# Optimization experiments

Measured on AMD Instinct MI355X. Metric: run time of the kernel, lower is better.

The kernel has to match this reference:

```python
import jax, jax.numpy as jnp
import numpy as np

N_NODES = 50000
N_EDGES = 1600000
IN_DIM = 128
HID = 128
SHARED = 64
N_GRAPHS = 2048


def setup_inputs() -> dict:
    key = jax.random.key(0)
    ks = jax.random.split(key, 16)
    x = jax.random.normal(ks[0], (N_NODES, IN_DIM), dtype=jnp.float32)
    edge_index = jax.random.randint(ks[1], (2, N_EDGES), 0, N_NODES, dtype=jnp.int64)
    batch = jnp.sort(jax.random.randint(ks[2], (N_NODES,), 0, N_GRAPHS, dtype=jnp.int64))

    def lin(k, fan_in, fan_out):
        bound = 1.0 / np.sqrt(fan_in)
        kw, kb = jax.random.split(k)
        W = jax.random.uniform(kw, (fan_in, fan_out), minval=-bound, maxval=bound, dtype=jnp.float32)
        b = jax.random.uniform(kb, (fan_out,), minval=-bound, maxval=bound, dtype=jnp.float32)
        return W, b

    W1a, b1a = lin(ks[3], IN_DIM, HID)
    W1b, b1b = lin(ks[4], HID, HID)
    W2a, b2a = lin(ks[5], HID, HID)
    W2b, b2b = lin(ks[6], HID, HID)
    Ws, bs = lin(ks[7], HID, SHARED)
    WlS, blS = lin(ks[8], SHARED, 1)
    WlP, blP = lin(ks[9], SHARED, 1)
    WnR, bnR = lin(ks[10], SHARED, 1)
    return dict(x=x, edge_index=edge_index, batch=batch,
                W1a=W1a, b1a=b1a, W1b=W1b, b1b=b1b,
                W2a=W2a, b2a=b2a, W2b=W2b, b2b=b2b,
                Ws=Ws, bs=bs, WlS=WlS, blS=blS, WlP=WlP, blP=blP, WnR=WnR, bnR=bnR)


def gin_conv(x, src, dst, Wa, ba, Wb, bb):
    # GINConv (eps=0): h_i = MLP(x_i + sum_{j->i} x_j)
    agg = jax.ops.segment_sum(x[src], dst, num_segments=N_NODES)
    h = x + agg
    h = jax.nn.relu(h @ Wa + ba)
    return h @ Wb + bb


def reference(x, edge_index, batch, W1a, b1a, W1b, b1b, W2a, b2a, W2b, b2b,
              Ws, bs, WlS, blS, WlP, blP, WnR, bnR):
    src, dst = edge_index[0], edge_index[1]
    h = jax.nn.relu(gin_conv(x, src, dst, W1a, b1a, W1b, b1b))
    h = jax.nn.relu(gin_conv(h, src, dst, W2a, b2a, W2b, b2b))
    # global mean pool over graph ids
    sums = jax.ops.segment_sum(h, batch, num_segments=N_GRAPHS)
    counts = jax.ops.segment_sum(jnp.ones((h.shape[0],), h.dtype), batch, num_segments=N_GRAPHS)
    pooled = sums / jnp.maximum(counts, 1.0)[:, None]
    g = jax.nn.relu(pooled @ Ws + bs)
    out_logS = (g @ WlS + blS)[:, 0]
    out_logP = (g @ WlP + blP)[:, 0]
    out_NR = (g @ WnR + bnR)[:, 0]
    return (out_logS, out_logP, out_NR)
```

## Files before the change

kernel.cpp:

```cpp
#include <hip/hip_runtime.h>
#include <hip/hip_bf16.h>


#define IN_DIM 128
#define NFINE 128
#define BIN_EPB 4096
#define SRCCH 16
#define NSLOT 6400
#define SPT 13

typedef float  f32x4  __attribute__((ext_vector_type(4)));
typedef short  bf16x4 __attribute__((ext_vector_type(4)));
typedef short  bf16x8 __attribute__((ext_vector_type(8)));

__device__ __forceinline__ unsigned short bf16_rne(float v) {
    unsigned u = __float_as_uint(v);
    unsigned t = u + 0x7fffu + ((u >> 16) & 1u);
    return (unsigned short)(t >> 16);
}


__global__ __launch_bounds__(256) void f32_to_bf16_kernel(
    const float4* __restrict__ in, uint4* __restrict__ out, int n8)
{
    int i = blockIdx.x * 256 + threadIdx.x;
    if (i >= n8) return;
    float4 a = in[i * 2];
    float4 b = in[i * 2 + 1];
    float v[8] = {a.x, a.y, a.z, a.w, b.x, b.y, b.z, b.w};
    unsigned r[4];
#pragma unroll
    for (int j = 0; j < 4; ++j)
        r[j] = (unsigned)bf16_rne(v[j * 2]) | ((unsigned)bf16_rne(v[j * 2 + 1]) << 16);
    out[i] = make_uint4(r[0], r[1], r[2], r[3]);
}


__global__ __launch_bounds__(256) void conv_weights_kernel(
    const float* __restrict__ W0, const float* __restrict__ W1,
    const float* __restrict__ W2, const float* __restrict__ W3,
    unsigned short* __restrict__ Wh, unsigned short* __restrict__ Wl)
{
    int m   = blockIdx.x >> 6;
    int idx = (blockIdx.x & 63) * 256 + threadIdx.x;
    const float* W = (m == 0) ? W0 : (m == 1) ? W1 : (m == 2) ? W2 : W3;
    int k = idx >> 7, n = idx & 127;
    float v = W[idx];
    unsigned short hh = bf16_rne(v);
    float hf = __uint_as_float(((unsigned)hh) << 16);
    unsigned short ll = bf16_rne(v - hf);
    Wh[m * 16384 + n * 128 + k] = hh;
    Wl[m * 16384 + n * 128 + k] = ll;
}


__global__ __launch_bounds__(256) void bin_kernel(
    const int* __restrict__ src, const int* __restrict__ dst,
    int2* __restrict__ buckets, int* __restrict__ bcur,
    int n_edges, int n_nodes, int cap)
{
    __shared__ int cnt[NFINE];
    __shared__ int base[NFINE];
    for (int i = threadIdx.x; i < NFINE; i += 256) cnt[i] = 0;
    __syncthreads();

    const int e0 = blockIdx.x * BIN_EPB + threadIdx.x * 16;
    int ne = n_edges - e0;
    if (ne < 0) ne = 0;
    if (ne > 16) ne = 16;

    int d[16], s[16], off[16];
    if (ne == 16) {
#pragma unroll
        for (int q = 0; q < 4; ++q) {
            int4 dv = *(const int4*)(dst + e0 + q * 4);
            int4 sv = *(const int4*)(src + e0 + q * 4);
            d[q * 4 + 0] = dv.x; d[q * 4 + 1] = dv.y;
            d[q * 4 + 2] = dv.z; d[q * 4 + 3] = dv.w;
            s[q * 4 + 0] = sv.x; s[q * 4 + 1] = sv.y;
            s[q * 4 + 2] = sv.z; s[q * 4 + 3] = sv.w;
        }
    } else {
#pragma unroll
        for (int j = 0; j < 16; ++j) {
            d[j] = (j < ne) ? dst[e0 + j] : 0;
            s[j] = (j < ne) ? src[e0 + j] : 0;
        }
    }
#pragma unroll
    for (int j = 0; j < 16; ++j)
        if (j < ne) {
            int b = (int)(((long long)d[j] * NFINE) / n_nodes);
            off[j] = atomicAdd(&cnt[b], 1);
        }
    __syncthreads();
    for (int i = threadIdx.x; i < NFINE; i += 256)
        base[i] = atomicAdd(&bcur[i], cnt[i]);
    __syncthreads();
#pragma unroll
    for (int j = 0; j < 16; ++j)
        if (j < ne) {
            int b = (int)(((long long)d[j] * NFINE) / n_nodes);
            buckets[(size_t)b * cap + base[b] + off[j]] = make_int2(d[j], s[j]);
        }
}

__global__ __launch_bounds__(512) void csr_fused_kernel(
    const int2* __restrict__ buckets, const int* __restrict__ bcnt,
    int* __restrict__ row_start, int* __restrict__ csr_src,
    int cap, int n_nodes, int n_edges)
{
    __shared__ int bc[NFINE];
    __shared__ int h[NSLOT];
    __shared__ int tsum[512];
    __shared__ int bbase_s;

    const int b = blockIdx.x;
    const int t = threadIdx.x;
    const int lo_n = (int)(((long long)b * n_nodes + NFINE - 1) / NFINE);
    const int hi_n = (int)(((long long)(b + 1) * n_nodes + NFINE - 1) / NFINE);
    const int sl = hi_n - lo_n;

    if (t < NFINE) bc[t] = bcnt[t];
    for (int i = t; i < NSLOT; i += 512) h[i] = 0;
    __syncthreads();
    if (t == 0) {
        int s = 0;
        for (int i = 0; i < b; ++i) s += bc[i];
        bbase_s = s;
    }
    const int nb = bc[b];
    const int2* bp = buckets + (size_t)b * cap;
    __syncthreads();

    for (int i = t; i < nb; i += 512) {
        int2 e = bp[i];
        int key = (e.x - lo_n) * SRCCH + (int)(((long long)e.y * SRCCH) / n_nodes);
        atomicAdd(&h[key], 1);
    }
    __syncthreads();

    int base = 0;
#pragma unroll
    for (int j = 0; j < SPT; ++j) {
        int slot = t * SPT + j;
        if (slot < NSLOT) {
            int v = h[slot];
            h[slot] = base;
            base += v;
        }
    }
    tsum[t] = base;
    __syncthreads();
    for (int off = 1; off < 512; off <<= 1) {
        int tmp = (t >= off) ? tsum[t - off] : 0;
        __syncthreads();
        tsum[t] += tmp;
        __syncthreads();
    }
    int texcl = tsum[t] - base + bbase_s;
#pragma unroll
    for (int j = 0; j < SPT; ++j) {
        int slot = t * SPT + j;
        if (slot < NSLOT) h[slot] += texcl;
    }
    __syncthreads();
    for (int i = t; i < sl; i += 512) row_start[lo_n + i] = h[i * SRCCH];
    if (b == NFINE - 1 && t == 0) row_start[n_nodes] = n_edges;
    __syncthreads();

    for (int i = t; i < nb; i += 512) {
        int2 e = bp[i];
        int key = (e.x - lo_n) * SRCCH + (int)(((long long)e.y * SRCCH) / n_nodes);
        csr_src[atomicAdd(&h[key], 1)] = e.y;
    }
}

#define HSTRIDE 132

__device__ __forceinline__ void add_row8(float acc[8], uint4 r) {
    union { unsigned u; float f; } c;
    c.u = r.x << 16;         acc[0] += c.f;
    c.u = r.x & 0xffff0000u; acc[1] += c.f;
    c.u = r.y << 16;         acc[2] += c.f;
    c.u = r.y & 0xffff0000u; acc[3] += c.f;
    c.u = r.z << 16;         acc[4] += c.f;
    c.u = r.z & 0xffff0000u; acc[5] += c.f;
    c.u = r.w << 16;         acc[6] += c.f;
    c.u = r.w & 0xffff0000u; acc[7] += c.f;
}

template <int LAYER>
__global__ __launch_bounds__(512) void fused_gin_layer_kernel(
    const float* __restrict__ xf,
    const uint4* __restrict__ selfh,
    const uint4* __restrict__ selfl,
    const uint4* __restrict__ nbr,
    const int* __restrict__ row_start, const int* __restrict__ csr_src,
    const unsigned short* __restrict__ Wa_h, const unsigned short* __restrict__ Wa_l,
    const float* __restrict__ ba,
    const unsigned short* __restrict__ Wb_h, const unsigned short* __restrict__ Wb_l,
    const float* __restrict__ bb,
    float* __restrict__ C, unsigned short* __restrict__ Ch,
    unsigned short* __restrict__ Cl, int M)
{
    __shared__ __align__(16) unsigned short Hh[64][HSTRIDE];
    __shared__ __align__(16) unsigned short Hl[64][HSTRIDE];

    const int t    = threadIdx.x;
    const int brow = blockIdx.x * 64;

    {
        const int lane = t & 15;
        const int gr   = t >> 4;
#pragma unroll
        for (int it = 0; it < 2; ++it) {
            const int rl   = it * 32 + gr;
            const int node = brow + rl;
            float acc[8] = {0.f, 0.f, 0.f, 0.f, 0.f, 0.f, 0.f, 0.f};
            if (node < M) {
                if constexpr (LAYER == 1) {
                    const f32x4* xfr = (const f32x4*)(xf + (size_t)node * IN_DIM + lane * 8);
                    f32x4 a0 = xfr[0];
                    f32x4 a1 = xfr[1];
                    acc[0] = a0.x; acc[1] = a0.y; acc[2] = a0.z; acc[3] = a0.w;
                    acc[4] = a1.x; acc[5] = a1.y; acc[6] = a1.z; acc[7] = a1.w;
                } else {
                    add_row8(acc, selfh[(size_t)node * 16 + lane]);
                    add_row8(acc, selfl[(size_t)node * 16 + lane]);
                }
                const int lo = row_start[node];
                const int hi = row_start[node + 1];
                int e = lo;
                for (; e + 3 < hi; e += 4) {
                    int s0 = csr_src[e];
                    int s1 = csr_src[e + 1];
                    int s2 = csr_src[e + 2];
                    int s3 = csr_src[e + 3];
                    uint4 r0 = nbr[(size_t)s0 * 16 + lane];
                    uint4 r1 = nbr[(size_t)s1 * 16 + lane];
                    uint4 r2 = nbr[(size_t)s2 * 16 + lane];
                    uint4 r3 = nbr[(size_t)s3 * 16 + lane];
                    add_row8(acc, r0);
                    add_row8(acc, r1);
                    add_row8(acc, r2);
                    add_row8(acc, r3);
                }
                for (; e < hi; ++e)
                    add_row8(acc, nbr[(size_t)csr_src[e] * 16 + lane]);
            }
            unsigned short hh[8], ll[8];
#pragma unroll
            for (int j = 0; j < 8; ++j) {
                unsigned short h = bf16_rne(acc[j]);
                hh[j] = h;
                ll[j] = bf16_rne(acc[j] - __uint_as_float(((unsigned)h) << 16));
            }
            *(bf16x4*)&Hh[rl][lane * 8]     = *(const bf16x4*)&hh[0];
            *(bf16x4*)&Hh[rl][lane * 8 + 4] = *(const bf16x4*)&hh[4];
            *(bf16x4*)&Hl[rl][lane * 8]     = *(const bf16x4*)&ll[0];
            *(bf16x4*)&Hl[rl][lane * 8 + 4] = *(const bf16x4*)&ll[4];
        }
    }
    __syncthreads();

    const int wave = t >> 6;
    const int lane = t & 63;
    const int l15  = lane & 15;
    const int quad = lane >> 4;
    const int rh   = (wave & 1) * 32;
    const int cq   = (wave >> 1) * 32;

    f32x4 acc[2][2];
#pragma unroll
    for (int ti = 0; ti < 2; ++ti)
#pragma unroll
        for (int ct = 0; ct < 2; ++ct) acc[ti][ct] = {0.f, 0.f, 0.f, 0.f};

#pragma unroll
    for (int k0 = 0; k0 < IN_DIM; k0 += 32) {
        const int hk = k0 + quad * 8;
        bf16x8 ah[2], al[2];
#pragma unroll
        for (int ti = 0; ti < 2; ++ti) {
            const int hr = rh + ti * 16 + l15;
            bf16x4 h0 = *(const bf16x4*)&Hh[hr][hk];
            bf16x4 h1 = *(const bf16x4*)&Hh[hr][hk + 4];
            bf16x4 l0 = *(const bf16x4*)&Hl[hr][hk];
            bf16x4 l1 = *(const bf16x4*)&Hl[hr][hk + 4];
            ah[ti] = __builtin_shufflevector(h0, h1, 0, 1, 2, 3, 4, 5, 6, 7);
            al[ti] = __builtin_shufflevector(l0, l1, 0, 1, 2, 3, 4, 5, 6, 7);
        }
#pragma unroll
        for (int ct = 0; ct < 2; ++ct) {
            const size_t woff = (size_t)(cq + ct * 16 + l15) * IN_DIM + k0 + quad * 8;
            bf16x8 wh = *(const bf16x8*)(Wa_h + woff);
            bf16x8 wl = *(const bf16x8*)(Wa_l + woff);
            acc[0][ct] = __builtin_amdgcn_mfma_f32_16x16x32_bf16(ah[0], wh, acc[0][ct], 0, 0, 0);
            acc[1][ct] = __builtin_amdgcn_mfma_f32_16x16x32_bf16(ah[1], wh, acc[1][ct], 0, 0, 0);
            acc[0][ct] = __builtin_amdgcn_mfma_f32_16x16x32_bf16(al[0], wh, acc[0][ct], 0, 0, 0);
            acc[1][ct] = __builtin_amdgcn_mfma_f32_16x16x32_bf16(al[1], wh, acc[1][ct], 0, 0, 0);
            acc[0][ct] = __builtin_amdgcn_mfma_f32_16x16x32_bf16(ah[0], wl, acc[0][ct], 0, 0, 0);
            acc[1][ct] = __builtin_amdgcn_mfma_f32_16x16x32_bf16(ah[1], wl, acc[1][ct], 0, 0, 0);
        }
    }
    __syncthreads();

#pragma unroll
    for (int ti = 0; ti < 2; ++ti) {
#pragma unroll
        for (int ct = 0; ct < 2; ++ct) {
            int col = cq + ct * 16 + l15;
            float b = ba[col];
#pragma unroll
            for (int r = 0; r < 4; ++r) {
                int rl = rh + ti * 16 + quad * 4 + r;
                float v = fmaxf(acc[ti][ct][r] + b, 0.f);
                unsigned short hh = bf16_rne(v);
                Hh[rl][col] = hh;
                Hl[rl][col] = bf16_rne(v - __uint_as_float(((unsigned)hh) << 16));
            }
            acc[ti][ct] = {0.f, 0.f, 0.f, 0.f};
        }
    }
    __syncthreads();

#pragma unroll
    for (int k0 = 0; k0 < IN_DIM; k0 += 32) {
        const int hk = k0 + quad * 8;
        bf16x8 ah[2], al[2];
#pragma unroll
        for (int ti = 0; ti < 2; ++ti) {
            const int hr = rh + ti * 16 + l15;
            bf16x4 h0 = *(const bf16x4*)&Hh[hr][hk];
            bf16x4 h1 = *(const bf16x4*)&Hh[hr][hk + 4];
            bf16x4 l0 = *(const bf16x4*)&Hl[hr][hk];
            bf16x4 l1 = *(const bf16x4*)&Hl[hr][hk + 4];
            ah[ti] = __builtin_shufflevector(h0, h1, 0, 1, 2, 3, 4, 5, 6, 7);
            al[ti] = __builtin_shufflevector(l0, l1, 0, 1, 2, 3, 4, 5, 6, 7);
        }
#pragma unroll
        for (int ct = 0; ct < 2; ++ct) {
            const size_t woff = (size_t)(cq + ct * 16 + l15) * IN_DIM + k0 + quad * 8;
            bf16x8 wh = *(const bf16x8*)(Wb_h + woff);
            bf16x8 wl = *(const bf16x8*)(Wb_l + woff);
            acc[0][ct] = __builtin_amdgcn_mfma_f32_16x16x32_bf16(ah[0], wh, acc[0][ct], 0, 0, 0);
            acc[1][ct] = __builtin_amdgcn_mfma_f32_16x16x32_bf16(ah[1], wh, acc[1][ct], 0, 0, 0);
            acc[0][ct] = __builtin_amdgcn_mfma_f32_16x16x32_bf16(al[0], wh, acc[0][ct], 0, 0, 0);
            acc[1][ct] = __builtin_amdgcn_mfma_f32_16x16x32_bf16(al[1], wh, acc[1][ct], 0, 0, 0);
            acc[0][ct] = __builtin_amdgcn_mfma_f32_16x16x32_bf16(ah[0], wl, acc[0][ct], 0, 0, 0);
            acc[1][ct] = __builtin_amdgcn_mfma_f32_16x16x32_bf16(ah[1], wl, acc[1][ct], 0, 0, 0);
        }
    }

#pragma unroll
    for (int ti = 0; ti < 2; ++ti) {
        const int rbase = brow + rh + ti * 16 + quad * 4;
#pragma unroll
        for (int ct = 0; ct < 2; ++ct) {
            int col = cq + ct * 16 + l15;
            float b = bb[col];
#pragma unroll
            for (int r = 0; r < 4; ++r) {
                int row = rbase + r;
                if (row < M) {
                    float o = fmaxf(acc[ti][ct][r] + b, 0.f);
                    if constexpr (LAYER == 1) {
                        unsigned short hh = bf16_rne(o);
                        Ch[(size_t)row * IN_DIM + col] = hh;
                        Cl[(size_t)row * IN_DIM + col] =
                            bf16_rne(o - __uint_as_float(((unsigned)hh) << 16));
                    } else {
                        C[(size_t)row * IN_DIM + col] = o;
                    }
                }
            }
        }
    }
}


__device__ __forceinline__ int lower_bound_i(const int* __restrict__ a, int n, int v) {
    int lo = 0, hi = n;
    while (lo < hi) {
        int mid = (lo + hi) >> 1;
        if (a[mid] < v) lo = mid + 1; else hi = mid;
    }
    return lo;
}

__global__ __launch_bounds__(128) void pool_kernel(
    const float* __restrict__ h, const int* __restrict__ batch,
    float* __restrict__ pooled, int n_nodes, int n_graphs)
{
    int g = blockIdx.x;
    int lo = lower_bound_i(batch, n_nodes, g);
    int hi = lower_bound_i(batch, n_nodes, g + 1);
    int j = threadIdx.x;
    float acc = 0.f;
    for (int i = lo; i < hi; ++i)
        acc += h[(size_t)i * IN_DIM + j];
    float cnt = (float)(hi - lo);
    pooled[(size_t)g * IN_DIM + j] = acc / fmaxf(cnt, 1.0f);
}

__global__ __launch_bounds__(64) void head_kernel(
    const float* __restrict__ pooled,
    const float* __restrict__ Ws,  const float* __restrict__ bs,
    const float* __restrict__ WlS, const float* __restrict__ blS,
    const float* __restrict__ WlP, const float* __restrict__ blP,
    const float* __restrict__ WnR, const float* __restrict__ bnR,
    float* __restrict__ out, int n_graphs)
{
    int g = blockIdx.x;
    int j = threadIdx.x;
    const float* p = pooled + (size_t)g * IN_DIM;
    float acc = bs[j];
#pragma unroll 8
    for (int k = 0; k < IN_DIM; ++k)
        acc = fmaf(p[k], Ws[k * 64 + j], acc);
    float gj = fmaxf(acc, 0.f);
    float s1 = gj * WlS[j];
    float s2 = gj * WlP[j];
    float s3 = gj * WnR[j];
#pragma unroll
    for (int off = 32; off > 0; off >>= 1) {
        s1 += __shfl_down(s1, off);
        s2 += __shfl_down(s2, off);
        s3 += __shfl_down(s3, off);
    }
    if (j == 0) {
        out[g]                = s1 + blS[0];
        out[n_graphs + g]     = s2 + blP[0];
        out[2 * n_graphs + g] = s3 + bnR[0];
    }
}


extern "C" void kernel_launch(void* const* d_in, const int* in_sizes, int n_in,
                              void* d_out, int out_size, void* d_ws, size_t ws_size,
                              hipStream_t stream)
{
    const float* x   = (const float*)d_in[0];
    const int*   ei  = (const int*)d_in[1];
    const int*   bat = (const int*)d_in[2];
    const float* W1a = (const float*)d_in[3];
    const float* b1a = (const float*)d_in[4];
    const float* W1b = (const float*)d_in[5];
    const float* b1b = (const float*)d_in[6];
    const float* W2a = (const float*)d_in[7];
    const float* b2a = (const float*)d_in[8];
    const float* W2b = (const float*)d_in[9];
    const float* b2b = (const float*)d_in[10];
    const float* Ws  = (const float*)d_in[11];
    const float* bs  = (const float*)d_in[12];
    const float* WlS = (const float*)d_in[13];
    const float* blS = (const float*)d_in[14];
    const float* WlP = (const float*)d_in[15];
    const float* blP = (const float*)d_in[16];
    const float* WnR = (const float*)d_in[17];
    const float* bnR = (const float*)d_in[18];

    const int n_nodes  = in_sizes[0] / IN_DIM;
    const int n_edges  = in_sizes[1] / 2;
    const int n_graphs = out_size / 3;
    const int* src = ei;
    const int* dst = ei + n_edges;

    const size_t node_elems   = (size_t)n_nodes * IN_DIM;
    const size_t pooled_elems = (size_t)n_graphs * IN_DIM;

    unsigned short* xb = (unsigned short*)d_ws;
    unsigned short* Ch = xb + node_elems;
    unsigned short* Cl = Ch + node_elems;
    float* P3     = (float*)(Cl + node_elems);
    float* pooled = P3 + node_elems;
    int* row_start = (int*)(pooled + pooled_elems);
    int* bcur      = row_start + (n_nodes + 1);
    int* csr_src   = bcur + NFINE;
    unsigned short* wt_h = (unsigned short*)(csr_src + n_edges);
    unsigned short* wt_l = wt_h + 4 * 16384;

    const int cap = n_edges / NFINE + 2048;
    int2* buckets = (int2*)P3;

    const int layerblocks = (n_nodes + 63) / 64;
    const int binblocks = (n_edges + BIN_EPB - 1) / BIN_EPB;
    const int n8 = (int)(node_elems / 8);
    const int cvtblocks = (n8 + 255) / 256;

    conv_weights_kernel<<<256, 256, 0, stream>>>(W1a, W1b, W2a, W2b, wt_h, wt_l);
    hipMemsetAsync(bcur, 0, NFINE * sizeof(int), stream);
    bin_kernel<<<binblocks, 256, 0, stream>>>(src, dst, buckets, bcur,
                                              n_edges, n_nodes, cap);
    csr_fused_kernel<<<NFINE, 512, 0, stream>>>(buckets, bcur, row_start,
                                                csr_src, cap, n_nodes, n_edges);
    f32_to_bf16_kernel<<<cvtblocks, 256, 0, stream>>>((const float4*)x, (uint4*)xb, n8);

    fused_gin_layer_kernel<1><<<layerblocks, 512, 0, stream>>>(
        x, nullptr, nullptr, (const uint4*)xb, row_start, csr_src,
        wt_h, wt_l, b1a, wt_h + 16384, wt_l + 16384, b1b,
        nullptr, Ch, Cl, n_nodes);

    fused_gin_layer_kernel<2><<<layerblocks, 512, 0, stream>>>(
        nullptr, (const uint4*)Ch, (const uint4*)Cl, (const uint4*)Ch,
        row_start, csr_src,
        wt_h + 2 * 16384, wt_l + 2 * 16384, b2a,
        wt_h + 3 * 16384, wt_l + 3 * 16384, b2b,
        P3, nullptr, nullptr, n_nodes);

    pool_kernel<<<n_graphs, 128, 0, stream>>>(P3, bat, pooled, n_nodes, n_graphs);
    head_kernel<<<n_graphs, 64, 0, stream>>>(pooled, Ws, bs, WlS, blS, WlP, blP,
                                             WnR, bnR, (float*)d_out, n_graphs);
}
```

Baseline: 344.0 us.

## Fuse mean-pool into layer-2 epilogue, merge setup kernels, double CSR bins

Layer 2 no longer writes a full fp32 node-feature array. Each block stages its output tile in LDS and does segmented column sums over the sorted batch ids, then atomically adds those sums into a zeroed pooled buffer. The count division moves into the head kernel, which finds graph boundaries by binary search. The weight conversion, x-to-bf16 conversion and memset are merged into one setup kernel, and the CSR binning changes from 128 to 256 fine buckets with smaller histograms. This removes one large write/read round trip and two launches, at the cost of float atomics that can make results nondeterministic.

```diff
diff --git a/kernel.cpp b/kernel.cpp
--- a/kernel.cpp
+++ b/kernel.cpp
@@ -3,11 +3,11 @@
 
 
 #define IN_DIM 128
-#define NFINE 128
+#define NFINE 256
 #define BIN_EPB 4096
 #define SRCCH 16
-#define NSLOT 6400
-#define SPT 13
+#define NSLOT 3200
+#define SPT 7
 
 typedef float  f32x4  __attribute__((ext_vector_type(4)));
 typedef short  bf16x4 __attribute__((ext_vector_type(4)));
@@ -20,37 +20,38 @@
 }
 
 
-__global__ __launch_bounds__(256) void f32_to_bf16_kernel(
-    const float4* __restrict__ in, uint4* __restrict__ out, int n8)
-{
-    int i = blockIdx.x * 256 + threadIdx.x;
-    if (i >= n8) return;
-    float4 a = in[i * 2];
-    float4 b = in[i * 2 + 1];
-    float v[8] = {a.x, a.y, a.z, a.w, b.x, b.y, b.z, b.w};
-    unsigned r[4];
-#pragma unroll
-    for (int j = 0; j < 4; ++j)
-        r[j] = (unsigned)bf16_rne(v[j * 2]) | ((unsigned)bf16_rne(v[j * 2 + 1]) << 16);
-    out[i] = make_uint4(r[0], r[1], r[2], r[3]);
-}
-
-
-__global__ __launch_bounds__(256) void conv_weights_kernel(
+__global__ __launch_bounds__(256) void setup_kernel(
+    const float4* __restrict__ xin, uint4* __restrict__ xb, int n8,
     const float* __restrict__ W0, const float* __restrict__ W1,
     const float* __restrict__ W2, const float* __restrict__ W3,
-    unsigned short* __restrict__ Wh, unsigned short* __restrict__ Wl)
+    unsigned short* __restrict__ Wh, unsigned short* __restrict__ Wl,
+    int* __restrict__ bcur, float* __restrict__ pooled, int npool)
 {
-    int m   = blockIdx.x >> 6;
-    int idx = (blockIdx.x & 63) * 256 + threadIdx.x;
-    const float* W = (m == 0) ? W0 : (m == 1) ? W1 : (m == 2) ? W2 : W3;
-    int k = idx >> 7, n = idx & 127;
-    float v = W[idx];
-    unsigned short hh = bf16_rne(v);
-    float hf = __uint_as_float(((unsigned)hh) << 16);
-    unsigned short ll = bf16_rne(v - hf);
-    Wh[m * 16384 + n * 128 + k] = hh;
-    Wl[m * 16384 + n * 128 + k] = ll;
+    int gid = blockIdx.x * 256 + threadIdx.x;
+    if (gid < n8) {
+        float4 a = xin[gid * 2];
+        float4 b = xin[gid * 2 + 1];
+        float v[8] = {a.x, a.y, a.z, a.w, b.x, b.y, b.z, b.w};
+        unsigned r[4];
+#pragma unroll
+        for (int j = 0; j < 4; ++j)
+            r[j] = (unsigned)bf16_rne(v[j * 2]) | ((unsigned)bf16_rne(v[j * 2 + 1]) << 16);
+        xb[gid] = make_uint4(r[0], r[1], r[2], r[3]);
+    }
+    if (gid < 4 * 16384) {
+        int m   = gid >> 14;
+        int idx = gid & 16383;
+        const float* W = (m == 0) ? W0 : (m == 1) ? W1 : (m == 2) ? W2 : W3;
+        int k = idx >> 7, n = idx & 127;
+        float v = W[idx];
+        unsigned short hh = bf16_rne(v);
+        float hf = __uint_as_float(((unsigned)hh) << 16);
+        unsigned short ll = bf16_rne(v - hf);
+        Wh[m * 16384 + n * 128 + k] = hh;
+        Wl[m * 16384 + n * 128 + k] = ll;
+    }
+    if (gid < NFINE) bcur[gid] = 0;
+    if (gid < npool) pooled[gid] = 0.f;
 }
 
 
@@ -121,7 +122,7 @@
     const int hi_n = (int)(((long long)(b + 1) * n_nodes + NFINE - 1) / NFINE);
     const int sl = hi_n - lo_n;
 
-    if (t < NFINE) bc[t] = bcnt[t];
+    for (int i = t; i < NFINE; i += 512) bc[i] = bcnt[i];
     for (int i = t; i < NSLOT; i += 512) h[i] = 0;
     __syncthreads();
     if (t == 0) {
@@ -201,11 +202,13 @@
     const float* __restrict__ ba,
     const unsigned short* __restrict__ Wb_h, const unsigned short* __restrict__ Wb_l,
     const float* __restrict__ bb,
-    float* __restrict__ C, unsigned short* __restrict__ Ch,
-    unsigned short* __restrict__ Cl, int M)
+    unsigned short* __restrict__ Ch, unsigned short* __restrict__ Cl,
+    float* __restrict__ pooled, const int* __restrict__ batch, int M)
 {
-    __shared__ __align__(16) unsigned short Hh[64][HSTRIDE];
-    __shared__ __align__(16) unsigned short Hl[64][HSTRIDE];
+    __shared__ __align__(16) unsigned short LDSBUF[2][64][HSTRIDE];
+    __shared__ int sbatch[64];
+    auto& Hh = LDSBUF[0];
+    auto& Hl = LDSBUF[1];
 
     const int t    = threadIdx.x;
     const int brow = blockIdx.x * 64;
@@ -353,28 +356,65 @@
         }
     }
 
-#pragma unroll
-    for (int ti = 0; ti < 2; ++ti) {
-        const int rbase = brow + rh + ti * 16 + quad * 4;
-#pragma unroll
-        for (int ct = 0; ct < 2; ++ct) {
-            int col = cq + ct * 16 + l15;
-            float b = bb[col];
-#pragma unroll
-            for (int r = 0; r < 4; ++r) {
-                int row = rbase + r;
-                if (row < M) {
-                    float o = fmaxf(acc[ti][ct][r] + b, 0.f);
-                    if constexpr (LAYER == 1) {
+    if constexpr (LAYER == 1) {
+#pragma unroll
+        for (int ti = 0; ti < 2; ++ti) {
+            const int rbase = brow + rh + ti * 16 + quad * 4;
+#pragma unroll
+            for (int ct = 0; ct < 2; ++ct) {
+                int col = cq + ct * 16 + l15;
+                float b = bb[col];
+#pragma unroll
+                for (int r = 0; r < 4; ++r) {
+                    int row = rbase + r;
+                    if (row < M) {
+                        float o = fmaxf(acc[ti][ct][r] + b, 0.f);
                         unsigned short hh = bf16_rne(o);
                         Ch[(size_t)row * IN_DIM + col] = hh;
                         Cl[(size_t)row * IN_DIM + col] =
                             bf16_rne(o - __uint_as_float(((unsigned)hh) << 16));
-                    } else {
-                        C[(size_t)row * IN_DIM + col] = o;
                     }
                 }
             }
+        }
+    } else {
+        __syncthreads();
+        float* ftile = (float*)&LDSBUF[0][0][0];
+#pragma unroll
+        for (int ti = 0; ti < 2; ++ti) {
+#pragma unroll
+            for (int ct = 0; ct < 2; ++ct) {
+                int col = cq + ct * 16 + l15;
+                float b = bb[col];
+#pragma unroll
+                for (int r = 0; r < 4; ++r) {
+                    int rl = rh + ti * 16 + quad * 4 + r;
+                    ftile[rl * 128 + col] = fmaxf(acc[ti][ct][r] + b, 0.f);
+                }
+            }
+        }
+        if (t < 64) {
+            int node = brow + t;
+            sbatch[t] = (node < M) ? batch[node] : -1;
+        }
+        __syncthreads();
+        if (t < 128) {
+            const int col = t;
+            float run = 0.f;
+            int curg = sbatch[0];
+#pragma unroll 1
+            for (int r = 0; r < 64; ++r) {
+                int g = sbatch[r];
+                if (g != curg) {
+                    if (curg >= 0)
+                        atomicAdd(&pooled[(size_t)curg * IN_DIM + col], run);
+                    curg = g;
+                    run = 0.f;
+                }
+                if (g >= 0) run += ftile[r * 128 + col];
+            }
+            if (curg >= 0)
+                atomicAdd(&pooled[(size_t)curg * IN_DIM + col], run);
         }
     }
 }
@@ -389,23 +429,8 @@
     return lo;
 }
 
-__global__ __launch_bounds__(128) void pool_kernel(
-    const float* __restrict__ h, const int* __restrict__ batch,
-    float* __restrict__ pooled, int n_nodes, int n_graphs)
-{
-    int g = blockIdx.x;
-    int lo = lower_bound_i(batch, n_nodes, g);
-    int hi = lower_bound_i(batch, n_nodes, g + 1);
-    int j = threadIdx.x;
-    float acc = 0.f;
-    for (int i = lo; i < hi; ++i)
-        acc += h[(size_t)i * IN_DIM + j];
-    float cnt = (float)(hi - lo);
-    pooled[(size_t)g * IN_DIM + j] = acc / fmaxf(cnt, 1.0f);
-}
-
 __global__ __launch_bounds__(64) void head_kernel(
-    const float* __restrict__ pooled,
+    const float* __restrict__ pooled, const int* __restrict__ batch, int n_nodes,
     const float* __restrict__ Ws,  const float* __restrict__ bs,
     const float* __restrict__ WlS, const float* __restrict__ blS,
     const float* __restrict__ WlP, const float* __restrict__ blP,
@@ -414,12 +439,15 @@
 {
     int g = blockIdx.x;
     int j = threadIdx.x;
+    int lo = lower_bound_i(batch, n_nodes, g);
+    int hi = lower_bound_i(batch, n_nodes, g + 1);
+    float inv = 1.f / fmaxf((float)(hi - lo), 1.0f);
     const float* p = pooled + (size_t)g * IN_DIM;
-    float acc = bs[j];
+    float acc = 0.f;
 #pragma unroll 8
     for (int k = 0; k < IN_DIM; ++k)
         acc = fmaf(p[k], Ws[k * 64 + j], acc);
-    float gj = fmaxf(acc, 0.f);
+    float gj = fmaxf(acc * inv + bs[j], 0.f);
     float s1 = gj * WlS[j];
     float s2 = gj * WlP[j];
     float s3 = gj * WnR[j];
@@ -473,8 +501,7 @@
     unsigned short* xb = (unsigned short*)d_ws;
     unsigned short* Ch = xb + node_elems;
     unsigned short* Cl = Ch + node_elems;
-    float* P3     = (float*)(Cl + node_elems);
-    float* pooled = P3 + node_elems;
+    float* pooled = (float*)(Cl + node_elems);
     int* row_start = (int*)(pooled + pooled_elems);
     int* bcur      = row_start + (n_nodes + 1);
     int* csr_src   = bcur + NFINE;
@@ -482,34 +509,34 @@
     unsigned short* wt_l = wt_h + 4 * 16384;
 
     const int cap = n_edges / NFINE + 2048;
-    int2* buckets = (int2*)P3;
+    int2* buckets = (int2*)Ch;
 
     const int layerblocks = (n_nodes + 63) / 64;
     const int binblocks = (n_edges + BIN_EPB - 1) / BIN_EPB;
     const int n8 = (int)(node_elems / 8);
     const int cvtblocks = (n8 + 255) / 256;
 
-    conv_weights_kernel<<<256, 256, 0, stream>>>(W1a, W1b, W2a, W2b, wt_h, wt_l);
-    hipMemsetAsync(bcur, 0, NFINE * sizeof(int), stream);
+    setup_kernel<<<cvtblocks, 256, 0, stream>>>(
+        (const float4*)x, (uint4*)xb, n8, W1a, W1b, W2a, W2b,
+        wt_h, wt_l, bcur, pooled, (int)pooled_elems);
     bin_kernel<<<binblocks, 256, 0, stream>>>(src, dst, buckets, bcur,
                                               n_edges, n_nodes, cap);
     csr_fused_kernel<<<NFINE, 512, 0, stream>>>(buckets, bcur, row_start,
                                                 csr_src, cap, n_nodes, n_edges);
-    f32_to_bf16_kernel<<<cvtblocks, 256, 0, stream>>>((const float4*)x, (uint4*)xb, n8);
 
     fused_gin_layer_kernel<1><<<layerblocks, 512, 0, stream>>>(
         x, nullptr, nullptr, (const uint4*)xb, row_start, csr_src,
         wt_h, wt_l, b1a, wt_h + 16384, wt_l + 16384, b1b,
-        nullptr, Ch, Cl, n_nodes);
+        Ch, Cl, nullptr, nullptr, n_nodes);
 
     fused_gin_layer_kernel<2><<<layerblocks, 512, 0, stream>>>(
         nullptr, (const uint4*)Ch, (const uint4*)Cl, (const uint4*)Ch,
         row_start, csr_src,
         wt_h + 2 * 16384, wt_l + 2 * 16384, b2a,
         wt_h + 3 * 16384, wt_l + 3 * 16384, b2b,
-        P3, nullptr, nullptr, n_nodes);
-
-    pool_kernel<<<n_graphs, 128, 0, stream>>>(P3, bat, pooled, n_nodes, n_graphs);
-    head_kernel<<<n_graphs, 64, 0, stream>>>(pooled, Ws, bs, WlS, blS, WlP, blP,
+        nullptr, nullptr, pooled, bat, n_nodes);
+
+    head_kernel<<<n_graphs, 64, 0, stream>>>(pooled, bat, n_nodes,
+                                             Ws, bs, WlS, blS, WlP, blP,
                                              WnR, bnR, (float*)d_out, n_graphs);
 }
```

New measurement: 319.9 us. -7.0%, faster.
